# Optimization experiments

Measured on AMD Instinct MI355X. Metric: run time of the kernel, lower is better.

Reference implementation:

```python
import jax, jax.numpy as jnp
import numpy as np

N = 1024      # total ROIs packed across the ragged batch
S = 14        # roi_output_size
C = 256       # conv_dim == feature_size
NC = 80       # num_classes
K = 4         # num_convs
DN = ('NHWC', 'HWIO', 'NHWC')


def setup_inputs() -> dict:
    key = jax.random.key(0)
    ks = jax.random.split(key, 5)
    x = jax.random.normal(ks[0], (N, S, S, C), jnp.float32)
    # 4 identical-shape 3x3 convs (C->C), stacked on a leading axis
    Wc = jax.random.normal(ks[1], (K, 3, 3, C, C), jnp.float32) * 0.03
    bc = jnp.zeros((K, C), jnp.float32)
    # 2x2 stride-2 transpose conv (C->C)
    Wt = jax.random.normal(ks[2], (2, 2, C, C), jnp.float32) * 0.03
    bt = jnp.zeros((C,), jnp.float32)
    # 1x1 mask predictor (C->NC), no activation
    Wm = jax.random.normal(ks[3], (1, 1, C, NC), jnp.float32) * 0.03
    bm = jnp.zeros((NC,), jnp.float32)
    return {"x": x, "Wc": Wc, "bc": bc, "Wt": Wt, "bt": bt, "Wm": Wm, "bm": bm}


def reference(x, Wc, bc, Wt, bt, Wm, bm):
    # Packed-batch equivalent of the nested tf.map_fn: conv math is
    # independent per ROI, so one batched conv over all ROIs is identical.
    for i in range(K):  # fixed small layer count
        x = jax.lax.conv_general_dilated(x, Wc[i], (1, 1), 'SAME', dimension_numbers=DN)
        x = jax.nn.relu(x + bc[i])
    # Conv2DTranspose(kernel=2, stride=2, padding='valid'), relu
    x = jax.lax.conv_transpose(x, Wt, (2, 2), 'VALID', dimension_numbers=DN)
    x = jax.nn.relu(x + bt)
    # 1x1 conv, linear activation -> [N, 28, 28, NC]
    x = jax.lax.conv_general_dilated(x, Wm, (1, 1), 'SAME', dimension_numbers=DN) + bm
    return x
```

## Files before the change

kernel.cpp:

```cpp
#include <hip/hip_runtime.h>


typedef _Float16 f16x8 __attribute__((ext_vector_type(8)));
typedef float    f32x4 __attribute__((ext_vector_type(4)));
typedef unsigned short u16;
typedef unsigned int   u32;

__device__ __forceinline__ u16 f2h(float f) {
  union { _Float16 h; u16 u; } c; c.h = (_Float16)f; return c.u;
}

__device__ __forceinline__ void store8(u16* dst, const u16* o) {
  uint4 v;
  v.x = (u32)o[0] | ((u32)o[1] << 16);
  v.y = (u32)o[2] | ((u32)o[3] << 16);
  v.z = (u32)o[4] | ((u32)o[5] << 16);
  v.w = (u32)o[6] | ((u32)o[7] << 16);
  *(uint4*)dst = v;
}

__global__ void prep_weights(const float* __restrict__ Wc, const float* __restrict__ Wt,
                             const float* __restrict__ Wm,
                             u16* __restrict__ WbP, u16* __restrict__ WtP,
                             u16* __restrict__ WmP) {
  int id = blockIdx.x * 256 + threadIdx.x;
  u16 o[8];
  if (id < 294912) {
    int li = id & 63; int rest = id >> 6;
    int ct = rest & 15; rest >>= 4;
    int kc = rest & 7;  rest >>= 3;
    int co  = ct * 16 + (li & 15);
    int ci0 = kc * 32 + (li >> 4) * 8;
#pragma unroll
    for (int j = 0; j < 8; j++) o[j] = f2h(Wc[(rest * 256 + ci0 + j) * 256 + co]);
    store8(&WbP[id * 8], o);
  } else if (id < 327680) {
    int id2 = id - 294912;
    int li = id2 & 63; int rest = id2 >> 6;
    int ct = rest & 15; rest >>= 4;
    int kc = rest & 7;  rest >>= 3;
    int srcq = 3 - rest;
    int co  = ct * 16 + (li & 15);
    int ci0 = kc * 32 + (li >> 4) * 8;
#pragma unroll
    for (int j = 0; j < 8; j++) o[j] = f2h(Wt[(srcq * 256 + ci0 + j) * 256 + co]);
    store8(&WtP[id2 * 8], o);
  } else if (id < 330240) {
    int id3 = id - 327680;
    int li = id3 & 63; int rest = id3 >> 6;
    int kc = rest / 5, nt = rest % 5;
    int nc  = nt * 16 + (li & 15);
    int ci0 = kc * 32 + (li >> 4) * 8;
#pragma unroll
    for (int j = 0; j < 8; j++) o[j] = f2h(Wm[(ci0 + j) * 80 + nc]);
    store8(&WmP[id3 * 8], o);
  }
}

template <bool INF32>
__global__ __launch_bounds__(256, 2)
void conv_layer(const void* __restrict__ in_, const u16* __restrict__ WbP,
                const float* __restrict__ bc, u16* __restrict__ out, int layer) {
  __shared__ u16 sA[196 * 136 + 128];
  const int ZP = 196 * 136;
  const int tid = threadIdx.x;
  const int w = tid >> 6, lane = tid & 63, q = lane >> 4, r = lane & 15;
  const int roi = blockIdx.x, mbase = blockIdx.y * 112;
  if (tid < 64) ((u32*)(sA + ZP))[tid] = 0u;

  int py[7], px[7];
#pragma unroll
  for (int mt = 0; mt < 7; mt++) {
    int p = mbase + mt * 16 + r;
    py[mt] = (p < 196) ? (p / 14) : 1000;
    px[mt] = p % 14;
  }
  f32x4 acc[7][4];
#pragma unroll
  for (int mt = 0; mt < 7; mt++)
#pragma unroll
    for (int nf = 0; nf < 4; nf++) acc[mt][nf] = (f32x4){0.f, 0.f, 0.f, 0.f};

  const float* xin = (const float*)in_;
  const u16*   yin = (const u16*)in_;

  for (int kh = 0; kh < 2; kh++) {
    if (kh) __syncthreads();
    if (INF32) {
      for (int c = tid; c < 196 * 32; c += 256) {
        int pix = c >> 5, c4 = (c & 31) * 4;
        const float4 v = *(const float4*)&xin[(roi * 196 + pix) * 256 + kh * 128 + c4];
        ushort4 h; h.x = f2h(v.x); h.y = f2h(v.y); h.z = f2h(v.z); h.w = f2h(v.w);
        *(ushort4*)&sA[pix * 136 + c4] = h;
      }
    } else {
      for (int c = tid; c < 196 * 16; c += 256) {
        int pix = c >> 4, c8 = (c & 15) * 8;
        *(uint4*)&sA[pix * 136 + c8] =
            *(const uint4*)&yin[(roi * 196 + pix) * 256 + kh * 128 + c8];
      }
    }
    __syncthreads();

    for (int tap = 0; tap < 9; tap++) {
      const int dy = tap / 3 - 1, dx = tap % 3 - 1;
      int offs[7];
#pragma unroll
      for (int mt = 0; mt < 7; mt++) {
        int ny = py[mt] + dy, nx = px[mt] + dx;
        bool v = ((u32)ny < 14u) && ((u32)nx < 14u);
        offs[mt] = v ? (ny * 14 + nx) * 136 : ZP;
      }
#pragma unroll
      for (int kk = 0; kk < 4; kk++) {
        const int kc = kh * 4 + kk;
        f16x8 b[4];
#pragma unroll
        for (int nf = 0; nf < 4; nf++)
          b[nf] = *(const f16x8*)&WbP[((((layer * 9 + tap) * 8 + kc) * 16 + (w * 4 + nf)) * 64 + lane) * 8];
#pragma unroll
        for (int mt = 0; mt < 7; mt++) {
          f16x8 a = *(const f16x8*)&sA[offs[mt] + kk * 32 + q * 8];
#pragma unroll
          for (int nf = 0; nf < 4; nf++)
            acc[mt][nf] = __builtin_amdgcn_mfma_f32_16x16x32_f16(a, b[nf], acc[mt][nf], 0, 0, 0);
        }
      }
    }
  }

  float bias[4];
#pragma unroll
  for (int nf = 0; nf < 4; nf++) bias[nf] = bc[layer * 256 + (w * 4 + nf) * 16 + r];
#pragma unroll
  for (int mt = 0; mt < 7; mt++) {
#pragma unroll
    for (int jj = 0; jj < 4; jj++) {
      int p = mbase + mt * 16 + q * 4 + jj;
      if (p < 196) {
#pragma unroll
        for (int nf = 0; nf < 4; nf++) {
          float v = acc[mt][nf][jj] + bias[nf];
          v = fmaxf(v, 0.f);
          out[(roi * 196 + p) * 256 + (w * 4 + nf) * 16 + r] = f2h(v);
        }
      }
    }
  }
}

__global__ __launch_bounds__(256, 2)
void tail_fused(const u16* __restrict__ y4, const u16* __restrict__ WtP,
                const u16* __restrict__ WmP, const float* __restrict__ bt,
                const float* __restrict__ bm, float* __restrict__ out) {
  __shared__ u16 sA[112 * 264 + 128];
  const int ZP = 112 * 264;
  const int tid = threadIdx.x;
  const int w = tid >> 6, lane = tid & 63, q = lane >> 4, r = lane & 15;
  const int roi = blockIdx.x, ab = blockIdx.y, mbase = blockIdx.z * 112;
  if (tid < 64) ((u32*)(sA + ZP))[tid] = 0u;

  int offs[7];
#pragma unroll
  for (int mt = 0; mt < 7; mt++) {
    int p = mbase + mt * 16 + r;
    offs[mt] = (p < 196) ? p * 136 : ZP;
  }
  f32x4 acc[7][4];
#pragma unroll
  for (int mt = 0; mt < 7; mt++)
#pragma unroll
    for (int nf = 0; nf < 4; nf++) acc[mt][nf] = (f32x4){0.f, 0.f, 0.f, 0.f};

  for (int kh = 0; kh < 2; kh++) {
    if (kh) __syncthreads();
    for (int c = tid; c < 196 * 16; c += 256) {
      int pix = c >> 4, c8 = (c & 15) * 8;
      *(uint4*)&sA[pix * 136 + c8] =
          *(const uint4*)&y4[(roi * 196 + pix) * 256 + kh * 128 + c8];
    }
    __syncthreads();
#pragma unroll
    for (int kk = 0; kk < 4; kk++) {
      const int kc = kh * 4 + kk;
      f16x8 b[4];
#pragma unroll
      for (int nf = 0; nf < 4; nf++)
        b[nf] = *(const f16x8*)&WtP[(((ab * 8 + kc) * 16 + (w * 4 + nf)) * 64 + lane) * 8];
#pragma unroll
      for (int mt = 0; mt < 7; mt++) {
        f16x8 a = *(const f16x8*)&sA[offs[mt] + kk * 32 + q * 8];
#pragma unroll
        for (int nf = 0; nf < 4; nf++)
          acc[mt][nf] = __builtin_amdgcn_mfma_f32_16x16x32_f16(a, b[nf], acc[mt][nf], 0, 0, 0);
      }
    }
  }

  __syncthreads();
  float btv[4];
#pragma unroll
  for (int nf = 0; nf < 4; nf++) btv[nf] = bt[(w * 4 + nf) * 16 + r];
#pragma unroll
  for (int mt = 0; mt < 7; mt++) {
#pragma unroll
    for (int jj = 0; jj < 4; jj++) {
      int row = mt * 16 + q * 4 + jj;
#pragma unroll
      for (int nf = 0; nf < 4; nf++) {
        float v = fmaxf(acc[mt][nf][jj] + btv[nf], 0.f);
        sA[row * 264 + (w * 4 + nf) * 16 + r] = f2h(v);
      }
    }
  }
  __syncthreads();

  float bmv[5];
#pragma unroll
  for (int nt = 0; nt < 5; nt++) bmv[nt] = bm[nt * 16 + r];
  const int a_ = ab >> 1, b_ = ab & 1;
  for (int tt = w; tt < 7; tt += 4) {
    f32x4 a2[5];
#pragma unroll
    for (int nt = 0; nt < 5; nt++) a2[nt] = (f32x4){0.f, 0.f, 0.f, 0.f};
#pragma unroll
    for (int kc = 0; kc < 8; kc++) {
      f16x8 af = *(const f16x8*)&sA[(tt * 16 + r) * 264 + kc * 32 + q * 8];
#pragma unroll
      for (int nt = 0; nt < 5; nt++) {
        f16x8 bw = *(const f16x8*)&WmP[((kc * 5 + nt) * 64 + lane) * 8];
        a2[nt] = __builtin_amdgcn_mfma_f32_16x16x32_f16(af, bw, a2[nt], 0, 0, 0);
      }
    }
#pragma unroll
    for (int jj = 0; jj < 4; jj++) {
      int row = tt * 16 + q * 4 + jj;
      int p = mbase + row;
      if (p < 196) {
        int y = p / 14, x = p % 14;
        int base = roi * 62720 + (2 * y + a_) * 2240 + (2 * x + b_) * 80;
#pragma unroll
        for (int nt = 0; nt < 5; nt++) out[base + nt * 16 + r] = a2[nt][jj] + bmv[nt];
      }
    }
  }
}

extern "C" void kernel_launch(void* const* d_in, const int* in_sizes, int n_in,
                              void* d_out, int out_size, void* d_ws, size_t ws_size,
                              hipStream_t stream) {
  const float* x  = (const float*)d_in[0];
  const float* Wc = (const float*)d_in[1];
  const float* bc = (const float*)d_in[2];
  const float* Wt = (const float*)d_in[3];
  const float* bt = (const float*)d_in[4];
  const float* Wm = (const float*)d_in[5];
  const float* bm = (const float*)d_in[6];
  float* out = (float*)d_out;

  char* ws = (char*)d_ws;
  u16* WbP = (u16*)(ws);
  u16* WtP = (u16*)(ws + 4718592);
  u16* WmP = (u16*)(ws + 5242880);
  u16* yA  = (u16*)(ws + 6291456);
  u16* yB  = (u16*)(ws + 6291456 + 102760448);

  prep_weights<<<1290, 256, 0, stream>>>(Wc, Wt, Wm, WbP, WtP, WmP);

  dim3 cg(1024, 2);
  conv_layer<true ><<<cg, 256, 0, stream>>>(x,  WbP, bc, yA, 0);
  conv_layer<false><<<cg, 256, 0, stream>>>(yA, WbP, bc, yB, 1);
  conv_layer<false><<<cg, 256, 0, stream>>>(yB, WbP, bc, yA, 2);
  conv_layer<false><<<cg, 256, 0, stream>>>(yA, WbP, bc, yB, 3);

  tail_fused<<<dim3(1024, 4, 2), 256, 0, stream>>>(yB, WtP, WmP, bt, bm, out);
}
```

Measured before the change: 1.709 ms.

## Halo-only LDS staging, double-buffered weight prefetch, and per-block tap rotation

Each conv block now stages only the input pixels it needs (its half of the ROI plus a halo row band) instead of all 196 pixels, which shrinks shared memory and cuts global loads. The tail kernel likewise loads only its own 112 or 84 pixels. Weight fragments are double-buffered in registers so the next k-chunk's B loads are issued before the current MFMAs run. The tap order is rotated per block to spread weight reads across the cache. The extra registers from the double buffer may reduce occupancy under the 2-waves launch bound.

```diff
diff --git a/kernel.cpp b/kernel.cpp
--- a/kernel.cpp
+++ b/kernel.cpp
@@ -61,11 +61,15 @@
 __global__ __launch_bounds__(256, 2)
 void conv_layer(const void* __restrict__ in_, const u16* __restrict__ WbP,
                 const float* __restrict__ bc, u16* __restrict__ out, int layer) {
-  __shared__ u16 sA[196 * 136 + 128];
-  const int ZP = 196 * 136;
+  __shared__ u16 sA[126 * 136 + 128];
+  const int ZP = 126 * 136;
   const int tid = threadIdx.x;
   const int w = tid >> 6, lane = tid & 63, q = lane >> 4, r = lane & 15;
-  const int roi = blockIdx.x, mbase = blockIdx.y * 112;
+  const int roi = blockIdx.x, mhalf = blockIdx.y;
+  const int mbase = mhalf * 112;
+  const int base_px = mhalf ? 98 : 0;
+  const int n_px   = mhalf ? 98 : 126;
+  const int rot = (blockIdx.x + mhalf) % 9;
   if (tid < 64) ((u32*)(sA + ZP))[tid] = 0u;
 
   int py[7], px[7];
@@ -84,46 +88,73 @@
   const float* xin = (const float*)in_;
   const u16*   yin = (const u16*)in_;
 
+  const u16* wb = WbP + (size_t)layer * 589824 + (w * 4) * 512 + lane * 8;
+
+  f16x8 b0[4], b1[4];
+#pragma unroll
+  for (int nf = 0; nf < 4; nf++)
+    b0[nf] = *(const f16x8*)&wb[rot * 65536 + nf * 512];
+
   for (int kh = 0; kh < 2; kh++) {
     if (kh) __syncthreads();
     if (INF32) {
-      for (int c = tid; c < 196 * 32; c += 256) {
+      for (int c = tid; c < n_px * 32; c += 256) {
         int pix = c >> 5, c4 = (c & 31) * 4;
-        const float4 v = *(const float4*)&xin[(roi * 196 + pix) * 256 + kh * 128 + c4];
+        const float4 v = *(const float4*)&xin[((size_t)roi * 196 + base_px + pix) * 256 + kh * 128 + c4];
         ushort4 h; h.x = f2h(v.x); h.y = f2h(v.y); h.z = f2h(v.z); h.w = f2h(v.w);
         *(ushort4*)&sA[pix * 136 + c4] = h;
       }
     } else {
-      for (int c = tid; c < 196 * 16; c += 256) {
+      for (int c = tid; c < n_px * 16; c += 256) {
         int pix = c >> 4, c8 = (c & 15) * 8;
         *(uint4*)&sA[pix * 136 + c8] =
-            *(const uint4*)&yin[(roi * 196 + pix) * 256 + kh * 128 + c8];
+            *(const uint4*)&yin[((size_t)roi * 196 + base_px + pix) * 256 + kh * 128 + c8];
       }
     }
     __syncthreads();
 
-    for (int tap = 0; tap < 9; tap++) {
+    for (int t = 0; t < 9; t++) {
+      int tap = t + rot; if (tap >= 9) tap -= 9;
       const int dy = tap / 3 - 1, dx = tap % 3 - 1;
       int offs[7];
 #pragma unroll
       for (int mt = 0; mt < 7; mt++) {
         int ny = py[mt] + dy, nx = px[mt] + dx;
         bool v = ((u32)ny < 14u) && ((u32)nx < 14u);
-        offs[mt] = v ? (ny * 14 + nx) * 136 : ZP;
+        offs[mt] = v ? ((ny * 14 + nx) - base_px) * 136 : ZP;
       }
 #pragma unroll
       for (int kk = 0; kk < 4; kk++) {
-        const int kc = kh * 4 + kk;
-        f16x8 b[4];
-#pragma unroll
-        for (int nf = 0; nf < 4; nf++)
-          b[nf] = *(const f16x8*)&WbP[((((layer * 9 + tap) * 8 + kc) * 16 + (w * 4 + nf)) * 64 + lane) * 8];
-#pragma unroll
-        for (int mt = 0; mt < 7; mt++) {
-          f16x8 a = *(const f16x8*)&sA[offs[mt] + kk * 32 + q * 8];
-#pragma unroll
-          for (int nf = 0; nf < 4; nf++)
-            acc[mt][nf] = __builtin_amdgcn_mfma_f32_16x16x32_f16(a, b[nf], acc[mt][nf], 0, 0, 0);
+        int nt = t, nh = kh, nk = kk + 1;
+        if (kk == 3) {
+          nk = 0; nt = t + 1;
+          if (nt == 9) {
+            if (kh == 0) { nt = 0; nh = 1; }
+            else         { nt = 8; nh = 1; nk = 3; }
+          }
+        }
+        int ntap = nt + rot; if (ntap >= 9) ntap -= 9;
+        const u16* wn = wb + (ntap * 8 + nh * 4 + nk) * 8192;
+        if ((kk & 1) == 0) {
+#pragma unroll
+          for (int nf = 0; nf < 4; nf++) b1[nf] = *(const f16x8*)&wn[nf * 512];
+#pragma unroll
+          for (int mt = 0; mt < 7; mt++) {
+            f16x8 a = *(const f16x8*)&sA[offs[mt] + kk * 32 + q * 8];
+#pragma unroll
+            for (int nf = 0; nf < 4; nf++)
+              acc[mt][nf] = __builtin_amdgcn_mfma_f32_16x16x32_f16(a, b0[nf], acc[mt][nf], 0, 0, 0);
+          }
+        } else {
+#pragma unroll
+          for (int nf = 0; nf < 4; nf++) b0[nf] = *(const f16x8*)&wn[nf * 512];
+#pragma unroll
+          for (int mt = 0; mt < 7; mt++) {
+            f16x8 a = *(const f16x8*)&sA[offs[mt] + kk * 32 + q * 8];
+#pragma unroll
+            for (int nf = 0; nf < 4; nf++)
+              acc[mt][nf] = __builtin_amdgcn_mfma_f32_16x16x32_f16(a, b1[nf], acc[mt][nf], 0, 0, 0);
+          }
         }
       }
     }
@@ -142,7 +173,7 @@
         for (int nf = 0; nf < 4; nf++) {
           float v = acc[mt][nf][jj] + bias[nf];
           v = fmaxf(v, 0.f);
-          out[(roi * 196 + p) * 256 + (w * 4 + nf) * 16 + r] = f2h(v);
+          out[((size_t)roi * 196 + p) * 256 + (w * 4 + nf) * 16 + r] = f2h(v);
         }
       }
     }
@@ -158,41 +189,58 @@
   const int tid = threadIdx.x;
   const int w = tid >> 6, lane = tid & 63, q = lane >> 4, r = lane & 15;
   const int roi = blockIdx.x, ab = blockIdx.y, mbase = blockIdx.z * 112;
+  const int n_px = mbase ? 84 : 112;
   if (tid < 64) ((u32*)(sA + ZP))[tid] = 0u;
 
   int offs[7];
 #pragma unroll
   for (int mt = 0; mt < 7; mt++) {
     int p = mbase + mt * 16 + r;
-    offs[mt] = (p < 196) ? p * 136 : ZP;
+    offs[mt] = (p < 196) ? (mt * 16 + r) * 136 : ZP;
   }
   f32x4 acc[7][4];
 #pragma unroll
   for (int mt = 0; mt < 7; mt++)
 #pragma unroll
     for (int nf = 0; nf < 4; nf++) acc[mt][nf] = (f32x4){0.f, 0.f, 0.f, 0.f};
+
+  const u16* wt = WtP + ab * 65536 + (w * 4) * 512 + lane * 8;
+  f16x8 b0[4], b1[4];
+#pragma unroll
+  for (int nf = 0; nf < 4; nf++) b0[nf] = *(const f16x8*)&wt[nf * 512];
 
   for (int kh = 0; kh < 2; kh++) {
     if (kh) __syncthreads();
-    for (int c = tid; c < 196 * 16; c += 256) {
+    for (int c = tid; c < n_px * 16; c += 256) {
       int pix = c >> 4, c8 = (c & 15) * 8;
       *(uint4*)&sA[pix * 136 + c8] =
-          *(const uint4*)&y4[(roi * 196 + pix) * 256 + kh * 128 + c8];
+          *(const uint4*)&y4[((size_t)roi * 196 + mbase + pix) * 256 + kh * 128 + c8];
     }
     __syncthreads();
 #pragma unroll
     for (int kk = 0; kk < 4; kk++) {
-      const int kc = kh * 4 + kk;
-      f16x8 b[4];
-#pragma unroll
-      for (int nf = 0; nf < 4; nf++)
-        b[nf] = *(const f16x8*)&WtP[(((ab * 8 + kc) * 16 + (w * 4 + nf)) * 64 + lane) * 8];
-#pragma unroll
-      for (int mt = 0; mt < 7; mt++) {
-        f16x8 a = *(const f16x8*)&sA[offs[mt] + kk * 32 + q * 8];
-#pragma unroll
-        for (int nf = 0; nf < 4; nf++)
-          acc[mt][nf] = __builtin_amdgcn_mfma_f32_16x16x32_f16(a, b[nf], acc[mt][nf], 0, 0, 0);
+      int nc_ = kh * 4 + kk + 1; if (nc_ > 7) nc_ = 7;
+      const u16* wn = wt + nc_ * 8192;
+      if ((kk & 1) == 0) {
+#pragma unroll
+        for (int nf = 0; nf < 4; nf++) b1[nf] = *(const f16x8*)&wn[nf * 512];
+#pragma unroll
+        for (int mt = 0; mt < 7; mt++) {
+          f16x8 a = *(const f16x8*)&sA[offs[mt] + kk * 32 + q * 8];
+#pragma unroll
+          for (int nf = 0; nf < 4; nf++)
+            acc[mt][nf] = __builtin_amdgcn_mfma_f32_16x16x32_f16(a, b0[nf], acc[mt][nf], 0, 0, 0);
+        }
+      } else {
+#pragma unroll
+        for (int nf = 0; nf < 4; nf++) b0[nf] = *(const f16x8*)&wn[nf * 512];
+#pragma unroll
+        for (int mt = 0; mt < 7; mt++) {
+          f16x8 a = *(const f16x8*)&sA[offs[mt] + kk * 32 + q * 8];
+#pragma unroll
+          for (int nf = 0; nf < 4; nf++)
+            acc[mt][nf] = __builtin_amdgcn_mfma_f32_16x16x32_f16(a, b1[nf], acc[mt][nf], 0, 0, 0);
+        }
       }
     }
   }
@@ -238,7 +286,7 @@
       int p = mbase + row;
       if (p < 196) {
         int y = p / 14, x = p % 14;
-        int base = roi * 62720 + (2 * y + a_) * 2240 + (2 * x + b_) * 80;
+        size_t base = (size_t)roi * 62720 + (2 * y + a_) * 2240 + (2 * x + b_) * 80;
 #pragma unroll
         for (int nt = 0; nt < 5; nt++) out[base + nt * 16 + r] = a2[nt][jj] + bmv[nt];
       }
```

After: 1.433 ms. -16.2%, faster.
